# Performance work log

Hardware: AMD Instinct MI355X
Metric: run time of the kernel (lower is better)

The kernel has to match this reference:

```python
import jax, jax.numpy as jnp
import numpy as np

EPS = 1e-8

def l2norm(x, axis=-1):
    norm = jnp.sqrt(jnp.sum(x * x, axis=axis, keepdims=True)) + EPS
    return x / norm

def setup_inputs() -> dict:
    key = jax.random.key(0)
    ks = jax.random.split(key, 4)
    B, Lq, Ls, d, sim_dim = 128, 128, 256, 1024, 256
    query = jax.random.normal(ks[0], (B, Lq, d), dtype=jnp.float32)
    context = jax.random.normal(ks[1], (B, Ls, d), dtype=jnp.float32)
    matrix = jax.random.uniform(ks[2], (B, Lq, d), dtype=jnp.float32)
    W = jax.random.normal(ks[3], (sim_dim, d), dtype=jnp.float32) * (1.0 / np.sqrt(d))
    b = jnp.zeros((sim_dim,), dtype=jnp.float32)
    smooth = 9
    return {"query": query, "context": context, "matrix": matrix, "W": W, "b": b, "smooth": smooth}

def reference(query, context, matrix, W, b, smooth):
    # cross_attention
    q = query * matrix                                   # (B, Lq, d)
    attn = jnp.einsum('bsd,bqd->bsq', context, q)        # (B, Ls, Lq)
    attn = jnp.where(attn >= 0, attn, 0.1 * attn)        # LeakyReLU(0.1)
    attn = l2norm(attn, axis=-1)                         # normalize over Lq
    attn = jnp.swapaxes(attn, 1, 2)                      # (B, Lq, Ls)
    attn = jax.nn.softmax(attn * smooth, axis=2)         # softmax over source
    wcontext = jnp.einsum('bqs,bsd->bqd', attn, context) # (B, Lq, d)
    wcontext = l2norm(wcontext, axis=-1)
    # alignment vector
    sim_rep = (query - wcontext) ** 2                    # (B, Lq, d)
    sim_rep = jnp.einsum('bqd,kd->bqk', sim_rep, W) + b  # Linear d -> sim_dim
    sim_rep = l2norm(sim_rep, axis=-1)
    return sim_rep
```

## Files before the change

### kernel.cpp

```cpp
#include <hip/hip_runtime.h>
#include <hip/hip_bf16.h>

constexpr int B  = 128;
constexpr int LQ = 128;
constexpr int LS = 256;
constexpr int D  = 1024;
constexpr int SD = 256;
constexpr float EPS = 1e-8f;

typedef __attribute__((ext_vector_type(8))) __bf16 bf16x8;
typedef __attribute__((ext_vector_type(4))) float f32x4;

__device__ inline ushort f2bf(float f) {
    union { float f; uint u; } v{f};
    uint r = v.u + 0x7fffu + ((v.u >> 16) & 1u);
    return (ushort)(r >> 16);
}
__device__ inline float bf2f(ushort u) {
    union { uint u; float f; } v{(uint)u << 16};
    return v.f;
}
__device__ inline uint4 pack8(float4 a, float4 b) {
    union { ushort us[8]; uint4 u4; } r;
    r.us[0]=f2bf(a.x); r.us[1]=f2bf(a.y); r.us[2]=f2bf(a.z); r.us[3]=f2bf(a.w);
    r.us[4]=f2bf(b.x); r.us[5]=f2bf(b.y); r.us[6]=f2bf(b.z); r.us[7]=f2bf(b.w);
    return r.u4;
}
__device__ inline int swz(int row, int kbyte) {
    return row * 128 + (kbyte ^ ((row & 7) << 4));
}
__device__ inline bf16x8 lds_frag(const ushort* base, int row, int kk, int lane) {
    int kbyte = kk * 64 + (lane >> 4) * 16;
    return *(const bf16x8*)((const char*)base + swz(row, kbyte));
}
__device__ inline int swz512(int row, int kbyte) {
    return row * 512 + (kbyte ^ ((row & 7) << 4));
}
__device__ inline f32x4 mfma16(bf16x8 a, bf16x8 b, f32x4 c) {
    return __builtin_amdgcn_mfma_f32_16x16x32_bf16(a, b, c, 0, 0, 0);
}

__global__ __launch_bounds__(256) void ctxT_kernel(
    const float* __restrict__ ctx, ushort* __restrict__ ctxT)
{
    const int b = blockIdx.z, d0 = blockIdx.x * 64, s0 = blockIdx.y * 64;
    __shared__ ushort T[64][72];
    const int t = threadIdx.x;
    const float* src = ctx + ((size_t)b * LS + s0) * D + d0;
    const int r = t >> 4;
    const int c = (t & 15) * 4;
#pragma unroll
    for (int p = 0; p < 4; ++p) {
        float4 v = *(const float4*)(src + (size_t)(r + p * 16) * D + c);
        T[c + 0][r + p * 16] = f2bf(v.x);
        T[c + 1][r + p * 16] = f2bf(v.y);
        T[c + 2][r + p * 16] = f2bf(v.z);
        T[c + 3][r + p * 16] = f2bf(v.w);
    }
    __syncthreads();
    ushort* dst = ctxT + ((size_t)b * D + d0) * LS + s0;
    const int rd = t >> 3;
    const int sc = (t & 7) * 8;
#pragma unroll
    for (int p = 0; p < 2; ++p) {
        uint4 o = *(const uint4*)&T[rd + p * 32][sc];
        *(uint4*)(dst + (size_t)(rd + p * 32) * LS + sc) = o;
    }
}

__global__ __launch_bounds__(256) void wconv_kernel(
    const float* __restrict__ W, ushort* __restrict__ Wb)
{
    size_t i = ((size_t)blockIdx.x * 256 + threadIdx.x) * 8;
    float4 a = *(const float4*)(W + i);
    float4 b = *(const float4*)(W + i + 4);
    *(uint4*)(Wb + i) = pack8(a, b);
}

__global__ __launch_bounds__(256) void qm_kernel(
    const float* __restrict__ query, const float* __restrict__ mat,
    ushort* __restrict__ qm)
{
    size_t i = ((size_t)blockIdx.x * 256 + threadIdx.x) * 8;
    float4 q1 = *(const float4*)(query + i), q2 = *(const float4*)(query + i + 4);
    float4 m1 = *(const float4*)(mat + i),   m2 = *(const float4*)(mat + i + 4);
    float4 p1{q1.x*m1.x, q1.y*m1.y, q1.z*m1.z, q1.w*m1.w};
    float4 p2{q2.x*m2.x, q2.y*m2.y, q2.z*m2.z, q2.w*m2.w};
    *(uint4*)(qm + i) = pack8(p1, p2);
}

__global__ __launch_bounds__(512) void gemmA_kernel(
    const ushort* __restrict__ qm, const float* __restrict__ ctx,
    const int* __restrict__ smooth_p, ushort* __restrict__ E)
{
    const int bid = blockIdx.x;
    const int xcd = bid & 7, idx = bid >> 3;
    const int b  = xcd * 16 + (idx >> 2);
    const int n0 = (idx & 3) * 64;
    __shared__ ushort As[2][128 * 64];
    __shared__ ushort Bs[2][64 * 64];
    __shared__ float colssP[2][64];
    __shared__ float invsm[64];
    const int t = threadIdx.x;
    const int wv = t >> 6, l = t & 63;
    const int wq = wv >> 2, wsv = wv & 3;

    const ushort* Ab = qm  + (size_t)b * LQ * D;
    const float*  Cb = ctx + ((size_t)b * LS + n0) * D;
    const int r0 = t >> 3, k8 = (t & 7) * 8;

    f32x4 acc[4] = {};
    uint4 a0, a1;
    float4 b0, b1;

    a0 = *(const uint4*)(Ab + (size_t)r0 * D + k8);
    a1 = *(const uint4*)(Ab + (size_t)(r0 + 64) * D + k8);
    b0 = *(const float4*)(Cb + (size_t)r0 * D + k8);
    b1 = *(const float4*)(Cb + (size_t)r0 * D + k8 + 4);
    *(uint4*)((char*)As[0] + swz(r0, k8 * 2))      = a0;
    *(uint4*)((char*)As[0] + swz(r0 + 64, k8 * 2)) = a1;
    *(uint4*)((char*)Bs[0] + swz(r0, k8 * 2))      = pack8(b0, b1);
    __syncthreads();

    int cur = 0;
#pragma unroll 1
    for (int ks = 0; ks < 15; ++ks) {
        const int k0 = (ks + 1) * 64;
        a0 = *(const uint4*)(Ab + (size_t)r0 * D + k0 + k8);
        a1 = *(const uint4*)(Ab + (size_t)(r0 + 64) * D + k0 + k8);
        b0 = *(const float4*)(Cb + (size_t)r0 * D + k0 + k8);
        b1 = *(const float4*)(Cb + (size_t)r0 * D + k0 + k8 + 4);
#pragma unroll
        for (int kk = 0; kk < 2; ++kk) {
            bf16x8 bfr = lds_frag(Bs[cur], wsv * 16 + (l & 15), kk, l);
#pragma unroll
            for (int i = 0; i < 4; ++i) {
                bf16x8 af = lds_frag(As[cur], wq * 64 + i * 16 + (l & 15), kk, l);
                acc[i] = mfma16(af, bfr, acc[i]);
            }
        }
        *(uint4*)((char*)As[cur ^ 1] + swz(r0, k8 * 2))      = a0;
        *(uint4*)((char*)As[cur ^ 1] + swz(r0 + 64, k8 * 2)) = a1;
        *(uint4*)((char*)Bs[cur ^ 1] + swz(r0, k8 * 2))      = pack8(b0, b1);
        __syncthreads();
        cur ^= 1;
    }
#pragma unroll
    for (int kk = 0; kk < 2; ++kk) {
        bf16x8 bfr = lds_frag(Bs[cur], wsv * 16 + (l & 15), kk, l);
#pragma unroll
        for (int i = 0; i < 4; ++i) {
            bf16x8 af = lds_frag(As[cur], wq * 64 + i * 16 + (l & 15), kk, l);
            acc[i] = mfma16(af, bfr, acc[i]);
        }
    }

    float csum = 0.f;
#pragma unroll
    for (int i = 0; i < 4; ++i)
#pragma unroll
        for (int r = 0; r < 4; ++r) {
            float v = acc[i][r];
            v = v >= 0.f ? v : 0.1f * v;
            acc[i][r] = v;
            csum += v * v;
        }
    csum += __shfl_xor(csum, 16);
    csum += __shfl_xor(csum, 32);
    if (l < 16) colssP[wq][wsv * 16 + l] = csum;
    __syncthreads();
    const float sm = (float)(*smooth_p);
    if (t < 64) invsm[t] = sm / (sqrtf(colssP[0][t] + colssP[1][t]) + EPS);
    __syncthreads();
    const float invc = invsm[wsv * 16 + (l & 15)];
    ushort* Eb = E + (size_t)b * LQ * LS + n0 + wsv * 16 + (l & 15);
#pragma unroll
    for (int i = 0; i < 4; ++i)
#pragma unroll
        for (int r = 0; r < 4; ++r) {
            int row = wq * 64 + i * 16 + (l >> 4) * 4 + r;
            Eb[(size_t)row * LS] = f2bf(__expf(acc[i][r] * invc));
        }
}

__global__ __launch_bounds__(512) void pv_kernel(
    const ushort* __restrict__ E, const ushort* __restrict__ ctxT,
    ushort* __restrict__ wctx, float* __restrict__ rowssP)
{
    const int bid = blockIdx.x;
    const int xcd = bid & 7, idx = bid >> 3;
    const int b  = xcd * 16 + (idx >> 2);
    const int qh = (idx >> 1) & 1, dh = idx & 1;
    __shared__ ushort Es[64 * 256];
    __shared__ ushort Bs[64 * 256];
    __shared__ float rsumL[64];
    __shared__ float rinv[64];
    __shared__ float rowssL[64][4];
    const int t = threadIdx.x;
    const int wv = t >> 6, l = t & 63;
    const int wq = wv >> 2, wd = wv & 3;
    const int cc = t & 31, rr = t >> 5;

    const ushort* Eb = E + ((size_t)b * LQ + qh * 64) * LS;
    float part[4];
#pragma unroll
    for (int it = 0; it < 4; ++it) {
        int row = rr + it * 16;
        uint4 v = *(const uint4*)(Eb + (size_t)row * LS + cc * 8);
        *(uint4*)((char*)Es + swz512(row, cc * 16)) = v;
        const ushort* us = (const ushort*)&v;
        float s = 0.f;
#pragma unroll
        for (int j = 0; j < 8; ++j) s += bf2f(us[j]);
        part[it] = s;
    }
    if (t < 256) rowssL[t >> 2][t & 3] = 0.f;
#pragma unroll
    for (int it = 0; it < 4; ++it) {
        float s = part[it];
        s += __shfl_xor(s, 1);  s += __shfl_xor(s, 2);
        s += __shfl_xor(s, 4);  s += __shfl_xor(s, 8);
        s += __shfl_xor(s, 16);
        if ((l & 31) == 0) rsumL[rr + it * 16] = s;
    }
    __syncthreads();
    if (t < 64) rinv[t] = 1.0f / rsumL[t];
    __syncthreads();

    bf16x8 af[2][8];
#pragma unroll
    for (int i = 0; i < 2; ++i)
#pragma unroll
        for (int kk = 0; kk < 8; ++kk)
            af[i][kk] = *(const bf16x8*)((const char*)Es +
                swz512(wq * 32 + i * 16 + (l & 15), kk * 64 + (l >> 4) * 16));

    const ushort* Cb = ctxT + ((size_t)b * D + dh * 512) * LS;
    ushort* Ob = wctx + ((size_t)b * LQ + qh * 64) * D + dh * 512;

#pragma unroll 1
    for (int dt = 0; dt < 8; ++dt) {
        __syncthreads();
#pragma unroll
        for (int it = 0; it < 4; ++it) {
            int row = rr + it * 16;
            uint4 v = *(const uint4*)(Cb + (size_t)(dt * 64 + row) * LS + cc * 8);
            *(uint4*)((char*)Bs + swz512(row, cc * 16)) = v;
        }
        __syncthreads();
        f32x4 acc[2] = {};
#pragma unroll
        for (int kk = 0; kk < 8; ++kk) {
            bf16x8 bfr = *(const bf16x8*)((const char*)Bs +
                swz512(wd * 16 + (l & 15), kk * 64 + (l >> 4) * 16));
            acc[0] = mfma16(af[0][kk], bfr, acc[0]);
            acc[1] = mfma16(af[1][kk], bfr, acc[1]);
        }
#pragma unroll
        for (int i = 0; i < 2; ++i)
#pragma unroll
            for (int r = 0; r < 4; ++r) {
                int row = wq * 32 + i * 16 + (l >> 4) * 4 + r;
                float wval = acc[i][r] * rinv[row];
                float p2 = wval * wval;
                p2 += __shfl_xor(p2, 1); p2 += __shfl_xor(p2, 2);
                p2 += __shfl_xor(p2, 4); p2 += __shfl_xor(p2, 8);
                if ((l & 15) == 0) rowssL[row][wd] += p2;
                Ob[(size_t)row * D + dt * 64 + wd * 16 + (l & 15)] = f2bf(wval);
            }
    }
    __syncthreads();
    if (t < 64)
        rowssP[(size_t)b * 256 + dh * 128 + qh * 64 + t] =
            rowssL[t][0] + rowssL[t][1] + rowssL[t][2] + rowssL[t][3];
}

__global__ __launch_bounds__(512) void gemm3_kernel(
    const ushort* __restrict__ wctx, const float* __restrict__ query,
    const float* __restrict__ rowssP, const ushort* __restrict__ Wb,
    const float* __restrict__ bias, float* __restrict__ out)
{
    const int m0 = blockIdx.x * 64;
    const int b  = blockIdx.y;
    __shared__ ushort As[64 * 64];
    __shared__ ushort Bs[256 * 64];
    __shared__ float red[64][4];
    __shared__ float invr[64];
    const int t = threadIdx.x;
    const int w = t >> 6, l = t & 63;
    const int wm = (w >> 2) * 32, wn = (w & 3) * 64;

    const int arow = t >> 3, ako = (t & 7) * 8;
    const float r0v = rowssP[(size_t)b * 256 + m0 + arow];
    const float r1v = rowssP[(size_t)b * 256 + 128 + m0 + arow];
    const float ivq = 1.0f / (sqrtf(r0v + r1v) + EPS);
    const float* Qp  = query + ((size_t)b * LQ + m0 + arow) * D + ako;
    const ushort* Wp = wctx  + ((size_t)b * LQ + m0 + arow) * D + ako;

    f32x4 acc[2][4] = {};

    for (int k0 = 0; k0 < D; k0 += 64) {
        if (k0) __syncthreads();
        {
            uint4 wu = *(const uint4*)(Wp + k0);
            float4 q1 = *(const float4*)(Qp + k0);
            float4 q2 = *(const float4*)(Qp + k0 + 4);
            float d0 = q1.x - bf2f((ushort)(wu.x & 0xffff)) * ivq;
            float d1 = q1.y - bf2f((ushort)(wu.x >> 16))    * ivq;
            float d2 = q1.z - bf2f((ushort)(wu.y & 0xffff)) * ivq;
            float d3 = q1.w - bf2f((ushort)(wu.y >> 16))    * ivq;
            float d4 = q2.x - bf2f((ushort)(wu.z & 0xffff)) * ivq;
            float d5 = q2.y - bf2f((ushort)(wu.z >> 16))    * ivq;
            float d6 = q2.z - bf2f((ushort)(wu.w & 0xffff)) * ivq;
            float d7 = q2.w - bf2f((ushort)(wu.w >> 16))    * ivq;
            float4 s1{d0*d0, d1*d1, d2*d2, d3*d3};
            float4 s2{d4*d4, d5*d5, d6*d6, d7*d7};
            *(uint4*)((char*)As + swz(arow, ako * 2)) = pack8(s1, s2);
        }
#pragma unroll
        for (int j = 0; j < 4; ++j) {
            int c = t + j * 512;
            int row = c >> 3, ko = (c & 7) * 8;
            *(uint4*)((char*)Bs + swz(row, ko * 2)) =
                *(const uint4*)(Wb + (size_t)row * D + k0 + ko);
        }
        __syncthreads();
#pragma unroll
        for (int kk = 0; kk < 2; ++kk) {
            bf16x8 af[2], bfr[4];
#pragma unroll
            for (int i = 0; i < 2; ++i) af[i] = lds_frag(As, wm + i * 16 + (l & 15), kk, l);
#pragma unroll
            for (int n = 0; n < 4; ++n) bfr[n] = lds_frag(Bs, wn + n * 16 + (l & 15), kk, l);
#pragma unroll
            for (int i = 0; i < 2; ++i)
#pragma unroll
                for (int n = 0; n < 4; ++n) acc[i][n] = mfma16(af[i], bfr[n], acc[i][n]);
        }
    }
#pragma unroll
    for (int n = 0; n < 4; ++n) {
        float bv = bias[wn + n * 16 + (l & 15)];
#pragma unroll
        for (int i = 0; i < 2; ++i)
#pragma unroll
            for (int r = 0; r < 4; ++r) acc[i][n][r] += bv;
    }
#pragma unroll
    for (int i = 0; i < 2; ++i)
#pragma unroll
        for (int r = 0; r < 4; ++r) {
            float p = 0.f;
#pragma unroll
            for (int n = 0; n < 4; ++n) p += acc[i][n][r] * acc[i][n][r];
#pragma unroll
            for (int off = 1; off < 16; off <<= 1) p += __shfl_xor(p, off);
            int rowl = wm + i * 16 + (l >> 4) * 4 + r;
            if ((l & 15) == 0) red[rowl][w & 3] = p;
        }
    __syncthreads();
    if (t < 64) {
        float s = red[t][0] + red[t][1] + red[t][2] + red[t][3];
        invr[t] = 1.0f / (sqrtf(s) + EPS);
    }
    __syncthreads();
    float* Ob = out + ((size_t)b * LQ + m0) * SD;
#pragma unroll
    for (int i = 0; i < 2; ++i)
#pragma unroll
        for (int r = 0; r < 4; ++r) {
            int rowl = wm + i * 16 + (l >> 4) * 4 + r;
            float iv = invr[rowl];
#pragma unroll
            for (int n = 0; n < 4; ++n) {
                int col = wn + n * 16 + (l & 15);
                Ob[(size_t)rowl * SD + col] = acc[i][n][r] * iv;
            }
        }
}

extern "C" void kernel_launch(void* const* d_in, const int* in_sizes, int n_in,
                              void* d_out, int out_size, void* d_ws, size_t ws_size,
                              hipStream_t stream)
{
    const float* query  = (const float*)d_in[0];
    const float* ctx    = (const float*)d_in[1];
    const float* mat    = (const float*)d_in[2];
    const float* W      = (const float*)d_in[3];
    const float* bias   = (const float*)d_in[4];
    const int*   smooth = (const int*)d_in[5];
    float* out = (float*)d_out;

    char* ws = (char*)d_ws;
    ushort* ctxT   = (ushort*)ws;
    ushort* qm     = (ushort*)(ws + (size_t)64 * 1024 * 1024);
    ushort* wctx   = qm;
    ushort* E      = (ushort*)(ws + (size_t)96 * 1024 * 1024);
    ushort* Wb     = (ushort*)(ws + (size_t)104 * 1024 * 1024);
    float*  rowssP = (float*)(ws + (size_t)(104 * 1024 + 512) * 1024);

    ctxT_kernel<<<dim3(D / 64, LS / 64, B), 256, 0, stream>>>(ctx, ctxT);
    wconv_kernel<<<dim3(SD * D / (256 * 8)), 256, 0, stream>>>(W, Wb);
    qm_kernel<<<dim3((size_t)B * LQ * D / (256 * 8)), 256, 0, stream>>>(query, mat, qm);
    gemmA_kernel<<<dim3(512), 512, 0, stream>>>(qm, ctx, smooth, E);
    pv_kernel<<<dim3(512), 512, 0, stream>>>(E, ctxT, wctx, rowssP);
    gemm3_kernel<<<dim3(2, B), 512, 0, stream>>>(wctx, query, rowssP, Wb, bias, out);
}
```

Measured before the change: 179.7 us.

## Fuse query*matrix product and context transpose into first GEMM kernel

```diff
diff --git a/kernel.cpp b/kernel.cpp
--- a/kernel.cpp
+++ b/kernel.cpp
@@ -38,34 +38,6 @@
 }
 __device__ inline f32x4 mfma16(bf16x8 a, bf16x8 b, f32x4 c) {
     return __builtin_amdgcn_mfma_f32_16x16x32_bf16(a, b, c, 0, 0, 0);
-}
-
-__global__ __launch_bounds__(256) void ctxT_kernel(
-    const float* __restrict__ ctx, ushort* __restrict__ ctxT)
-{
-    const int b = blockIdx.z, d0 = blockIdx.x * 64, s0 = blockIdx.y * 64;
-    __shared__ ushort T[64][72];
-    const int t = threadIdx.x;
-    const float* src = ctx + ((size_t)b * LS + s0) * D + d0;
-    const int r = t >> 4;
-    const int c = (t & 15) * 4;
-#pragma unroll
-    for (int p = 0; p < 4; ++p) {
-        float4 v = *(const float4*)(src + (size_t)(r + p * 16) * D + c);
-        T[c + 0][r + p * 16] = f2bf(v.x);
-        T[c + 1][r + p * 16] = f2bf(v.y);
-        T[c + 2][r + p * 16] = f2bf(v.z);
-        T[c + 3][r + p * 16] = f2bf(v.w);
-    }
-    __syncthreads();
-    ushort* dst = ctxT + ((size_t)b * D + d0) * LS + s0;
-    const int rd = t >> 3;
-    const int sc = (t & 7) * 8;
-#pragma unroll
-    for (int p = 0; p < 2; ++p) {
-        uint4 o = *(const uint4*)&T[rd + p * 32][sc];
-        *(uint4*)(dst + (size_t)(rd + p * 32) * LS + sc) = o;
-    }
 }
 
 __global__ __launch_bounds__(256) void wconv_kernel(
@@ -77,21 +49,10 @@
     *(uint4*)(Wb + i) = pack8(a, b);
 }
 
-__global__ __launch_bounds__(256) void qm_kernel(
+__global__ __launch_bounds__(512) void gemmA_kernel(
     const float* __restrict__ query, const float* __restrict__ mat,
-    ushort* __restrict__ qm)
-{
-    size_t i = ((size_t)blockIdx.x * 256 + threadIdx.x) * 8;
-    float4 q1 = *(const float4*)(query + i), q2 = *(const float4*)(query + i + 4);
-    float4 m1 = *(const float4*)(mat + i),   m2 = *(const float4*)(mat + i + 4);
-    float4 p1{q1.x*m1.x, q1.y*m1.y, q1.z*m1.z, q1.w*m1.w};
-    float4 p2{q2.x*m2.x, q2.y*m2.y, q2.z*m2.z, q2.w*m2.w};
-    *(uint4*)(qm + i) = pack8(p1, p2);
-}
-
-__global__ __launch_bounds__(512) void gemmA_kernel(
-    const ushort* __restrict__ qm, const float* __restrict__ ctx,
-    const int* __restrict__ smooth_p, ushort* __restrict__ E)
+    const float* __restrict__ ctx, const int* __restrict__ smooth_p,
+    ushort* __restrict__ E, ushort* __restrict__ ctxT)
 {
     const int bid = blockIdx.x;
     const int xcd = bid & 7, idx = bid >> 3;
@@ -105,31 +66,55 @@
     const int wv = t >> 6, l = t & 63;
     const int wq = wv >> 2, wsv = wv & 3;
 
-    const ushort* Ab = qm  + (size_t)b * LQ * D;
-    const float*  Cb = ctx + ((size_t)b * LS + n0) * D;
+    const float* Qb = query + (size_t)b * LQ * D;
+    const float* Mb = mat   + (size_t)b * LQ * D;
+    const float* Cb = ctx   + ((size_t)b * LS + n0) * D;
     const int r0 = t >> 3, k8 = (t & 7) * 8;
 
+    const int ed = t >> 3;
+    const int es = (t & 7) * 8;
+    ushort* CTb = ctxT + (size_t)b * D * LS + n0 + es;
+
     f32x4 acc[4] = {};
-    uint4 a0, a1;
-    float4 b0, b1;
-
-    a0 = *(const uint4*)(Ab + (size_t)r0 * D + k8);
-    a1 = *(const uint4*)(Ab + (size_t)(r0 + 64) * D + k8);
-    b0 = *(const float4*)(Cb + (size_t)r0 * D + k8);
-    b1 = *(const float4*)(Cb + (size_t)r0 * D + k8 + 4);
-    *(uint4*)((char*)As[0] + swz(r0, k8 * 2))      = a0;
-    *(uint4*)((char*)As[0] + swz(r0 + 64, k8 * 2)) = a1;
-    *(uint4*)((char*)Bs[0] + swz(r0, k8 * 2))      = pack8(b0, b1);
+    float4 q0, q1, q2, q3, m0, m1, m2, m3, c0, c1;
+
+    {
+        const float* qp = Qb + (size_t)r0 * D + k8;
+        const float* mp = Mb + (size_t)r0 * D + k8;
+        q0 = *(const float4*)qp;  q1 = *(const float4*)(qp + 4);
+        m0 = *(const float4*)mp;  m1 = *(const float4*)(mp + 4);
+        qp += (size_t)64 * D;  mp += (size_t)64 * D;
+        q2 = *(const float4*)qp;  q3 = *(const float4*)(qp + 4);
+        m2 = *(const float4*)mp;  m3 = *(const float4*)(mp + 4);
+        const float* cp = Cb + (size_t)r0 * D + k8;
+        c0 = *(const float4*)cp;  c1 = *(const float4*)(cp + 4);
+    }
+    {
+        float4 p1{q0.x*m0.x, q0.y*m0.y, q0.z*m0.z, q0.w*m0.w};
+        float4 p2{q1.x*m1.x, q1.y*m1.y, q1.z*m1.z, q1.w*m1.w};
+        *(uint4*)((char*)As[0] + swz(r0, k8 * 2)) = pack8(p1, p2);
+        float4 p3{q2.x*m2.x, q2.y*m2.y, q2.z*m2.z, q2.w*m2.w};
+        float4 p4{q3.x*m3.x, q3.y*m3.y, q3.z*m3.z, q3.w*m3.w};
+        *(uint4*)((char*)As[0] + swz(r0 + 64, k8 * 2)) = pack8(p3, p4);
+        *(uint4*)((char*)Bs[0] + swz(r0, k8 * 2)) = pack8(c0, c1);
+    }
     __syncthreads();
 
     int cur = 0;
 #pragma unroll 1
     for (int ks = 0; ks < 15; ++ks) {
         const int k0 = (ks + 1) * 64;
-        a0 = *(const uint4*)(Ab + (size_t)r0 * D + k0 + k8);
-        a1 = *(const uint4*)(Ab + (size_t)(r0 + 64) * D + k0 + k8);
-        b0 = *(const float4*)(Cb + (size_t)r0 * D + k0 + k8);
-        b1 = *(const float4*)(Cb + (size_t)r0 * D + k0 + k8 + 4);
+        {
+            const float* qp = Qb + (size_t)r0 * D + k0 + k8;
+            const float* mp = Mb + (size_t)r0 * D + k0 + k8;
+            q0 = *(const float4*)qp;  q1 = *(const float4*)(qp + 4);
+            m0 = *(const float4*)mp;  m1 = *(const float4*)(mp + 4);
+            qp += (size_t)64 * D;  mp += (size_t)64 * D;
+            q2 = *(const float4*)qp;  q3 = *(const float4*)(qp + 4);
+            m2 = *(const float4*)mp;  m3 = *(const float4*)(mp + 4);
+            const float* cp = Cb + (size_t)r0 * D + k0 + k8;
+            c0 = *(const float4*)cp;  c1 = *(const float4*)(cp + 4);
+        }
 #pragma unroll
         for (int kk = 0; kk < 2; ++kk) {
             bf16x8 bfr = lds_frag(Bs[cur], wsv * 16 + (l & 15), kk, l);
@@ -139,9 +124,23 @@
                 acc[i] = mfma16(af, bfr, acc[i]);
             }
         }
-        *(uint4*)((char*)As[cur ^ 1] + swz(r0, k8 * 2))      = a0;
-        *(uint4*)((char*)As[cur ^ 1] + swz(r0 + 64, k8 * 2)) = a1;
-        *(uint4*)((char*)Bs[cur ^ 1] + swz(r0, k8 * 2))      = pack8(b0, b1);
+        {
+            uint4 tv;
+            ushort* tp = (ushort*)&tv;
+#pragma unroll
+            for (int j = 0; j < 8; ++j)
+                tp[j] = *(const ushort*)((const char*)Bs[cur] + swz(es + j, ed * 2));
+            *(uint4*)(CTb + (size_t)(ks * 64 + ed) * LS) = tv;
+        }
+        {
+            float4 p1{q0.x*m0.x, q0.y*m0.y, q0.z*m0.z, q0.w*m0.w};
+            float4 p2{q1.x*m1.x, q1.y*m1.y, q1.z*m1.z, q1.w*m1.w};
+            *(uint4*)((char*)As[cur ^ 1] + swz(r0, k8 * 2)) = pack8(p1, p2);
+            float4 p3{q2.x*m2.x, q2.y*m2.y, q2.z*m2.z, q2.w*m2.w};
+            float4 p4{q3.x*m3.x, q3.y*m3.y, q3.z*m3.z, q3.w*m3.w};
+            *(uint4*)((char*)As[cur ^ 1] + swz(r0 + 64, k8 * 2)) = pack8(p3, p4);
+            *(uint4*)((char*)Bs[cur ^ 1] + swz(r0, k8 * 2)) = pack8(c0, c1);
+        }
         __syncthreads();
         cur ^= 1;
     }
@@ -153,6 +152,14 @@
             bf16x8 af = lds_frag(As[cur], wq * 64 + i * 16 + (l & 15), kk, l);
             acc[i] = mfma16(af, bfr, acc[i]);
         }
+    }
+    {
+        uint4 tv;
+        ushort* tp = (ushort*)&tv;
+#pragma unroll
+        for (int j = 0; j < 8; ++j)
+            tp[j] = *(const ushort*)((const char*)Bs[cur] + swz(es + j, ed * 2));
+        *(uint4*)(CTb + (size_t)(15 * 64 + ed) * LS) = tv;
     }
 
     float csum = 0.f;
@@ -393,16 +400,13 @@
 
     char* ws = (char*)d_ws;
     ushort* ctxT   = (ushort*)ws;
-    ushort* qm     = (ushort*)(ws + (size_t)64 * 1024 * 1024);
-    ushort* wctx   = qm;
+    ushort* wctx   = (ushort*)(ws + (size_t)64 * 1024 * 1024);
     ushort* E      = (ushort*)(ws + (size_t)96 * 1024 * 1024);
     ushort* Wb     = (ushort*)(ws + (size_t)104 * 1024 * 1024);
     float*  rowssP = (float*)(ws + (size_t)(104 * 1024 + 512) * 1024);
 
-    ctxT_kernel<<<dim3(D / 64, LS / 64, B), 256, 0, stream>>>(ctx, ctxT);
     wconv_kernel<<<dim3(SD * D / (256 * 8)), 256, 0, stream>>>(W, Wb);
-    qm_kernel<<<dim3((size_t)B * LQ * D / (256 * 8)), 256, 0, stream>>>(query, mat, qm);
-    gemmA_kernel<<<dim3(512), 512, 0, stream>>>(qm, ctx, smooth, E);
+    gemmA_kernel<<<dim3(512), 512, 0, stream>>>(query, mat, ctx, smooth, E, ctxT);
     pv_kernel<<<dim3(512), 512, 0, stream>>>(E, ctxT, wctx, rowssP);
     gemm3_kernel<<<dim3(2, B), 512, 0, stream>>>(wctx, query, rowssP, Wb, bias, out);
 }
```

Measured after the change: 162.8 us. -9.4%, faster.
